# Kernel optimization log

Hardware: AMD Instinct MI355X
Metric: run time of the kernel (lower is better)

## Reference

```python
import jax, jax.numpy as jnp
import numpy as np

BN_EPS = 1e-5

def conv1x1(x, w, b):
    # x: [B, Cin, L], w: [Cout, Cin], b: [Cout] -> [B, Cout, L]
    return jnp.einsum('bcl,oc->bol', x, w) + b[None, :, None]

def maxpool2(x):
    # x: [B, C, L] -> [B, C, L//2], kernel=stride=2
    B, C, L = x.shape
    return x.reshape(B, C, L // 2, 2).max(axis=-1)

def setup_inputs() -> dict:
    key = jax.random.key(0)
    ks = jax.random.split(key, 12)
    B, C, L = 8, 512, 4096
    Ci = C // 2
    s_in = 1.0 / np.sqrt(C)
    s_mid = 1.0 / np.sqrt(Ci)
    return {
        'x':       jax.random.normal(ks[0], (B, C, L), jnp.float32),
        'theta_w': jax.random.uniform(ks[1], (Ci, C), jnp.float32, -s_in, s_in),
        'theta_b': jax.random.uniform(ks[2], (Ci,), jnp.float32, -s_in, s_in),
        'phi_w':   jax.random.uniform(ks[3], (Ci, C), jnp.float32, -s_in, s_in),
        'phi_b':   jax.random.uniform(ks[4], (Ci,), jnp.float32, -s_in, s_in),
        'g_w':     jax.random.uniform(ks[5], (Ci, C), jnp.float32, -s_in, s_in),
        'g_b':     jax.random.uniform(ks[6], (Ci,), jnp.float32, -s_in, s_in),
        'wz_w':    jax.random.uniform(ks[7], (C, Ci), jnp.float32, -s_mid, s_mid),
        'wz_b':    jax.random.uniform(ks[8], (C,), jnp.float32, -s_mid, s_mid),
        'bn_gamma': jax.random.normal(ks[9], (C,), jnp.float32),
        'bn_beta':  jax.random.normal(ks[10], (C,), jnp.float32),
    }

def reference(x, theta_w, theta_b, phi_w, phi_b, g_w, g_b, wz_w, wz_b, bn_gamma, bn_beta):
    B, C, L = x.shape
    Ci = C // 2
    # projections
    theta = conv1x1(x, theta_w, theta_b)                 # [B, Ci, L]
    phi   = maxpool2(conv1x1(x, phi_w, phi_b))           # [B, Ci, L/2]
    g     = maxpool2(conv1x1(x, g_w, g_b))               # [B, Ci, L/2]
    # non-local attention (unscaled)
    f = jnp.einsum('bcq,bck->bqk', theta, phi)           # [B, L, L/2]
    f = jax.nn.softmax(f, axis=-1)
    y = jnp.einsum('bqk,bck->bcq', f, g)                 # [B, Ci, L]
    # wz: conv1x1 + BatchNorm1d (training mode: batch stats, biased var)
    z = conv1x1(y, wz_w, wz_b)                           # [B, C, L]
    mean = z.mean(axis=(0, 2))
    var = ((z - mean[None, :, None]) ** 2).mean(axis=(0, 2))
    z_hat = (z - mean[None, :, None]) * jax.lax.rsqrt(var + BN_EPS)[None, :, None]
    wz = z_hat * bn_gamma[None, :, None] + bn_beta[None, :, None]
    return wz + x
```

## Files before the change

### kernel.cpp

```cpp
#include <hip/hip_runtime.h>

#define BATCH 8
#define CIN   512
#define LEN   4096
#define CI    256
#define KLEN  2048

typedef _Float16 half_t;
typedef _Float16 half2_t __attribute__((ext_vector_type(2)));
typedef _Float16 half4_t __attribute__((ext_vector_type(4)));
typedef _Float16 half8_t __attribute__((ext_vector_type(8)));
typedef float    floatx4 __attribute__((ext_vector_type(4)));

__device__ __forceinline__ void async16(void* lds_dst, const void* g_src) {
    __builtin_amdgcn_global_load_lds(
        (const __attribute__((address_space(1))) unsigned int*)g_src,
        (__attribute__((address_space(3))) unsigned int*)lds_dst,
        16, 0, 0);
}

__global__ __launch_bounds__(256) void xpose_kernel(
    const float* __restrict__ x, half_t* __restrict__ xhT)
{
    __shared__ half_t tile[64][72];
    const int b = blockIdx.z, c0 = blockIdx.y * 64, l0 = blockIdx.x * 64;
    const int t = threadIdx.x;
    #pragma unroll
    for (int i = 0; i < 4; i++) {
        int fid = t + 256 * i;
        int c = fid >> 4, lb = (fid & 15) << 2;
        float4 v = *(const float4*)(x + ((size_t)b * CIN + c0 + c) * LEN + l0 + lb);
        tile[lb + 0][c] = (half_t)v.x;
        tile[lb + 1][c] = (half_t)v.y;
        tile[lb + 2][c] = (half_t)v.z;
        tile[lb + 3][c] = (half_t)v.w;
    }
    __syncthreads();
    #pragma unroll
    for (int i = 0; i < 2; i++) {
        int fid = t + 256 * i;
        int l = fid >> 3, cb = (fid & 7) << 3;
        half8_t v = *(const half8_t*)&tile[l][cb];
        *(half8_t*)(xhT + ((size_t)b * LEN + l0 + l) * CIN + c0 + cb) = v;
    }
}

__global__ __launch_bounds__(256) void wconv_kernel(
    const float* __restrict__ tw, const float* __restrict__ pw,
    const float* __restrict__ gw, const float* __restrict__ wzw,
    half_t* __restrict__ Wh, half_t* __restrict__ wzh)
{
    size_t base = ((size_t)blockIdx.x * 256 + threadIdx.x) * 8;
    const float* src;
    half_t* dst;
    if (base < 768 * 512) {
        size_t o = base >> 9, c = base & 511;
        src = (o < 256 ? tw + o * 512
                       : (o < 512 ? pw + (o - 256) * 512 : gw + (o - 512) * 512)) + c;
        dst = Wh + base;
    } else {
        size_t off = base - 768 * 512;
        src = wzw + off;
        dst = wzh + off;
    }
    float4 a = *(const float4*)src, b2 = *(const float4*)(src + 4);
    half8_t h = { (half_t)a.x, (half_t)a.y, (half_t)a.z, (half_t)a.w,
                  (half_t)b2.x, (half_t)b2.y, (half_t)b2.z, (half_t)b2.w };
    *(half8_t*)dst = h;
}

__global__ __launch_bounds__(256, 2) void projmm_kernel(
    const half_t* __restrict__ xhT, const half_t* __restrict__ Wh,
    const float* __restrict__ tb, const float* __restrict__ pb,
    const float* __restrict__ gb,
    half_t* __restrict__ thetaT, half_t* __restrict__ phiT,
    half_t* __restrict__ gperm)
{
    __shared__ half_t wsm[128 * 32];
    __shared__ half_t xsm[128 * 32];

    const int b  = blockIdx.z;
    const int o0 = blockIdx.y * 128;
    const int l0 = blockIdx.x * 128;
    const int t  = threadIdx.x;
    const int lane = t & 63, w = t >> 6;
    const int ln = lane & 15, quad = lane >> 4;
    const int wm = w >> 1, wn = w & 1;

    floatx4 acc[4][4];
    #pragma unroll
    for (int mi = 0; mi < 4; mi++)
        #pragma unroll
        for (int nj = 0; nj < 4; nj++) acc[mi][nj] = (floatx4)(0.0f);

    const half_t* Wb = Wh + (size_t)o0 * 512;
    const half_t* xb = xhT + ((size_t)b * LEN + l0) * CIN;

    for (int k0 = 0; k0 < 512; k0 += 32) {
        __syncthreads();
        #pragma unroll
        for (int it = 0; it < 2; it++) {
            int grp = w * 2 + it;
            async16(&wsm[grp * 512],
                    Wb + (size_t)(grp * 16 + ln) * 512 + k0 + quad * 8);
            async16(&xsm[grp * 512],
                    xb + (size_t)(grp * 16 + ln) * CIN + k0 + quad * 8);
        }
        __syncthreads();
        half8_t af[4], bf[4];
        #pragma unroll
        for (int mi = 0; mi < 4; mi++)
            af[mi] = *(const half8_t*)&wsm[(wm * 4 + mi) * 512 + lane * 8];
        #pragma unroll
        for (int nj = 0; nj < 4; nj++)
            bf[nj] = *(const half8_t*)&xsm[(wn * 4 + nj) * 512 + lane * 8];
        #pragma unroll
        for (int mi = 0; mi < 4; mi++)
            #pragma unroll
            for (int nj = 0; nj < 4; nj++)
                acc[mi][nj] = __builtin_amdgcn_mfma_f32_16x16x32_f16(
                                  af[mi], bf[nj], acc[mi][nj], 0, 0, 0);
    }

    const int which = o0 >> 8;
    const int obase = o0 & 255;
    const float* Bp = which == 0 ? tb : (which == 1 ? pb : gb);

    float bias[4][4];
    #pragma unroll
    for (int mi = 0; mi < 4; mi++)
        #pragma unroll
        for (int r = 0; r < 4; r++)
            bias[mi][r] = Bp[obase + wm * 64 + mi * 16 + quad * 4 + r];

    if (which == 0) {
        #pragma unroll
        for (int mi = 0; mi < 4; mi++) {
            int o = obase + wm * 64 + mi * 16 + quad * 4;
            #pragma unroll
            for (int nj = 0; nj < 4; nj++) {
                int l = l0 + wn * 64 + nj * 16 + ln;
                half4_t v = { (half_t)(acc[mi][nj][0] + bias[mi][0]),
                              (half_t)(acc[mi][nj][1] + bias[mi][1]),
                              (half_t)(acc[mi][nj][2] + bias[mi][2]),
                              (half_t)(acc[mi][nj][3] + bias[mi][3]) };
                *(half4_t*)(thetaT + ((size_t)b * LEN + l) * CI + o) = v;
            }
        }
    } else {
        #pragma unroll
        for (int mi = 0; mi < 4; mi++) {
            int o = obase + wm * 64 + mi * 16 + quad * 4;
            #pragma unroll
            for (int nj = 0; nj < 4; nj++) {
                int l = l0 + wn * 64 + nj * 16 + ln;
                float mx[4];
                #pragma unroll
                for (int r = 0; r < 4; r++) {
                    float other = __shfl_xor(acc[mi][nj][r], 1);
                    mx[r] = fmaxf(acc[mi][nj][r], other) + bias[mi][r];
                }
                if ((ln & 1) == 0) {
                    int kk = l >> 1;
                    if (which == 1) {
                        half4_t v = { (half_t)mx[0], (half_t)mx[1],
                                      (half_t)mx[2], (half_t)mx[3] };
                        *(half4_t*)(phiT + ((size_t)b * KLEN + kk) * CI + o) = v;
                    } else {
                        int loc = kk & 63;
                        int v = ((loc >> 5) & 1) * 32 + ((loc >> 2) & 3) * 8
                              + ((loc >> 4) & 1) * 4 + (loc & 3);
                        int kdst = (kk & ~63) | v;
                        #pragma unroll
                        for (int r = 0; r < 4; r++)
                            gperm[((size_t)b * CI + o + r) * KLEN + kdst] =
                                (half_t)mx[r];
                    }
                }
            }
        }
    }
}

__global__ __launch_bounds__(256, 2) void attn_kernel(
    const half_t* __restrict__ thetaT,
    const half_t* __restrict__ phiT,
    const half_t* __restrict__ gperm,
    half_t* __restrict__ yhT)
{
    __shared__ half_t phi_s[64 * 256];
    __shared__ half_t g_s[256 * 64];

    const int b    = blockIdx.x;
    const int q0   = blockIdx.y * 64;
    const int t    = threadIdx.x;
    const int w    = t >> 6;
    const int lane = t & 63;
    const int ln   = lane & 15;
    const int quad = lane >> 4;
    const int qw   = q0 + w * 16;

    half8_t thf[8];
    {
        const half_t* thb = thetaT + ((size_t)b * LEN + qw + ln) * CI + quad * 8;
        #pragma unroll
        for (int ch = 0; ch < 8; ch++)
            thf[ch] = *(const half8_t*)(thb + ch * 32);
    }

    floatx4 O[16];
    #pragma unroll
    for (int i = 0; i < 16; i++) O[i] = (floatx4)(0.0f);
    float m_run = -3.0e38f;
    float l_run = 0.0f;

    const half_t* phib = phiT + (size_t)b * KLEN * CI;
    const half_t* gpb  = gperm + (size_t)b * CI * KLEN;

    for (int kt = 0; kt < KLEN; kt += 64) {
        __syncthreads();
        #pragma unroll
        for (int ii = 0; ii < 8; ii++) {
            int grp = w * 8 + ii;
            int k16 = grp >> 3, ch = grp & 7;
            async16(&phi_s[grp * 512],
                    phib + (size_t)(kt + k16 * 16 + ln) * CI + ch * 32 + quad * 8);
        }
        #pragma unroll
        for (int ii = 0; ii < 8; ii++) {
            int grp = w * 8 + ii;
            int tc = grp >> 4, csub = grp & 15;
            async16(&g_s[grp * 512],
                    gpb + (size_t)(csub * 16 + ln) * KLEN + kt + tc * 32 + quad * 8);
        }
        __syncthreads();

        floatx4 S[4];
        #pragma unroll
        for (int k16 = 0; k16 < 4; k16++) S[k16] = (floatx4)(0.0f);
        #pragma unroll
        for (int k16 = 0; k16 < 4; k16++)
            #pragma unroll
            for (int ch = 0; ch < 8; ch++) {
                half8_t a = *(const half8_t*)&phi_s[(k16 * 8 + ch) * 512 + lane * 8];
                S[k16] = __builtin_amdgcn_mfma_f32_16x16x32_f16(
                             a, thf[ch], S[k16], 0, 0, 0);
            }

        float tmax = S[0][0];
        #pragma unroll
        for (int k16 = 0; k16 < 4; k16++)
            #pragma unroll
            for (int r = 0; r < 4; r++) tmax = fmaxf(tmax, S[k16][r]);
        tmax = fmaxf(tmax, __shfl_xor(tmax, 16));
        tmax = fmaxf(tmax, __shfl_xor(tmax, 32));
        float m_new = fmaxf(m_run, tmax);
        float alpha = __expf(m_run - m_new);
        m_run = m_new;
        l_run *= alpha;

        float p[4][4];
        #pragma unroll
        for (int k16 = 0; k16 < 4; k16++) {
            #pragma unroll
            for (int r = 0; r < 4; r++) {
                p[k16][r] = __expf(S[k16][r] - m_new);
                l_run += p[k16][r];
            }
        }
        half8_t Pf[2];
        #pragma unroll
        for (int tc = 0; tc < 2; tc++) {
            half8_t pv = { (half_t)p[2*tc][0],   (half_t)p[2*tc][1],
                           (half_t)p[2*tc][2],   (half_t)p[2*tc][3],
                           (half_t)p[2*tc+1][0], (half_t)p[2*tc+1][1],
                           (half_t)p[2*tc+1][2], (half_t)p[2*tc+1][3] };
            Pf[tc] = pv;
        }
        #pragma unroll
        for (int i = 0; i < 16; i++) O[i] *= alpha;

        #pragma unroll
        for (int tc = 0; tc < 2; tc++)
            #pragma unroll
            for (int csub = 0; csub < 16; csub++) {
                half8_t a = *(const half8_t*)&g_s[(tc * 16 + csub) * 512 + lane * 8];
                O[csub] = __builtin_amdgcn_mfma_f32_16x16x32_f16(
                              a, Pf[tc], O[csub], 0, 0, 0);
            }
    }

    l_run += __shfl_xor(l_run, 16);
    l_run += __shfl_xor(l_run, 32);
    float inv = 1.0f / l_run;
    half_t* yb = yhT + ((size_t)b * LEN + qw + ln) * CI;
    #pragma unroll
    for (int csub = 0; csub < 16; csub++) {
        int c = csub * 16 + quad * 4;
        half4_t v = { (half_t)(O[csub][0] * inv), (half_t)(O[csub][1] * inv),
                      (half_t)(O[csub][2] * inv), (half_t)(O[csub][3] * inv) };
        *(half4_t*)(yb + c) = v;
    }
}

__global__ __launch_bounds__(256, 2) void zmm_kernel(
    const half_t* __restrict__ yhT, const half_t* __restrict__ wzh,
    const float* __restrict__ wzb, float* __restrict__ z,
    float* __restrict__ bns, float* __restrict__ bnq)
{
    __shared__ half_t ysm[128 * 32];
    __shared__ half_t wsm[128 * 32];

    const int b  = blockIdx.z;
    const int o0 = blockIdx.y * 128;
    const int l0 = blockIdx.x * 128;
    const int t  = threadIdx.x;
    const int lane = t & 63, w = t >> 6;
    const int ln = lane & 15, quad = lane >> 4;
    const int wm = w >> 1, wn = w & 1;

    floatx4 acc[4][4];
    #pragma unroll
    for (int mi = 0; mi < 4; mi++)
        #pragma unroll
        for (int nj = 0; nj < 4; nj++) acc[mi][nj] = (floatx4)(0.0f);

    const half_t* yb = yhT + ((size_t)b * LEN + l0) * CI;
    const half_t* Wb = wzh + (size_t)o0 * CI;

    for (int k0 = 0; k0 < 256; k0 += 32) {
        __syncthreads();
        #pragma unroll
        for (int it = 0; it < 2; it++) {
            int grp = w * 2 + it;
            async16(&ysm[grp * 512],
                    yb + (size_t)(grp * 16 + ln) * CI + k0 + quad * 8);
            async16(&wsm[grp * 512],
                    Wb + (size_t)(grp * 16 + ln) * CI + k0 + quad * 8);
        }
        __syncthreads();
        half8_t af[4], bf[4];
        #pragma unroll
        for (int mi = 0; mi < 4; mi++)
            af[mi] = *(const half8_t*)&ysm[(wm * 4 + mi) * 512 + lane * 8];
        #pragma unroll
        for (int nj = 0; nj < 4; nj++)
            bf[nj] = *(const half8_t*)&wsm[(wn * 4 + nj) * 512 + lane * 8];
        #pragma unroll
        for (int mi = 0; mi < 4; mi++)
            #pragma unroll
            for (int nj = 0; nj < 4; nj++)
                acc[mi][nj] = __builtin_amdgcn_mfma_f32_16x16x32_f16(
                                  af[mi], bf[nj], acc[mi][nj], 0, 0, 0);
    }

    float s[4] = {0, 0, 0, 0}, s2[4] = {0, 0, 0, 0};
    #pragma unroll
    for (int nj = 0; nj < 4; nj++) {
        int o = o0 + wn * 64 + nj * 16 + ln;
        float bo = wzb[o];
        #pragma unroll
        for (int mi = 0; mi < 4; mi++) {
            int l = l0 + wm * 64 + mi * 16 + quad * 4;
            float4 v = make_float4(acc[mi][nj][0] + bo, acc[mi][nj][1] + bo,
                                   acc[mi][nj][2] + bo, acc[mi][nj][3] + bo);
            *(float4*)(z + ((size_t)b * CIN + o) * LEN + l) = v;
            s[nj]  += (v.x + v.y) + (v.z + v.w);
            s2[nj] += (v.x * v.x + v.y * v.y) + (v.z * v.z + v.w * v.w);
        }
    }
    #pragma unroll
    for (int nj = 0; nj < 4; nj++) {
        float sv = s[nj], qv = s2[nj];
        sv += __shfl_xor(sv, 16); sv += __shfl_xor(sv, 32);
        qv += __shfl_xor(qv, 16); qv += __shfl_xor(qv, 32);
        if (quad == 0) {
            int o = o0 + wn * 64 + nj * 16 + ln;
            atomicAdd(&bns[o], sv);
            atomicAdd(&bnq[o], qv);
        }
    }
}

__global__ __launch_bounds__(256) void bn_kernel(
    float* __restrict__ z, const float* __restrict__ x,
    const float* __restrict__ bns, const float* __restrict__ bnq,
    const float* __restrict__ gamma, const float* __restrict__ beta)
{
    size_t i4 = (size_t)blockIdx.x * 256 + threadIdx.x;
    size_t base = i4 << 2;
    int c = (int)((base >> 12) & (CIN - 1));
    const float invn = 1.0f / (BATCH * LEN);
    float mean = bns[c] * invn;
    float var  = bnq[c] * invn - mean * mean;
    float sc = gamma[c] * rsqrtf(var + 1e-5f);
    float sh = beta[c] - mean * sc;
    float4 zv = *(const float4*)(z + base);
    float4 xv = *(const float4*)(x + base);
    float4 o;
    o.x = zv.x * sc + sh + xv.x;
    o.y = zv.y * sc + sh + xv.y;
    o.z = zv.z * sc + sh + xv.z;
    o.w = zv.w * sc + sh + xv.w;
    *(float4*)(z + base) = o;
}

extern "C" void kernel_launch(void* const* d_in, const int* in_sizes, int n_in,
                              void* d_out, int out_size, void* d_ws, size_t ws_size,
                              hipStream_t stream)
{
    const float* x     = (const float*)d_in[0];
    const float* tw    = (const float*)d_in[1];
    const float* tb    = (const float*)d_in[2];
    const float* pw    = (const float*)d_in[3];
    const float* pb    = (const float*)d_in[4];
    const float* gw    = (const float*)d_in[5];
    const float* gb    = (const float*)d_in[6];
    const float* wzw   = (const float*)d_in[7];
    const float* wzb   = (const float*)d_in[8];
    const float* gamma = (const float*)d_in[9];
    const float* beta  = (const float*)d_in[10];

    float* out = (float*)d_out;

    half_t* xhT    = (half_t*)d_ws;
    half_t* thetaT = xhT    + (size_t)BATCH * LEN * CIN;
    half_t* phiT   = thetaT + (size_t)BATCH * LEN * CI;
    half_t* gperm  = phiT   + (size_t)BATCH * KLEN * CI;
    half_t* yhT    = gperm  + (size_t)BATCH * CI * KLEN;
    half_t* Wh     = yhT    + (size_t)BATCH * LEN * CI;
    half_t* wzh    = Wh     + (size_t)768 * 512;
    float*  bns    = (float*)(wzh + (size_t)512 * 256);
    float*  bnq    = bns + CIN;

    hipMemsetAsync(bns, 0, 2 * CIN * sizeof(float), stream);

    wconv_kernel<<<256, 256, 0, stream>>>(tw, pw, gw, wzw, Wh, wzh);

    xpose_kernel<<<dim3(LEN / 64, CIN / 64, BATCH), 256, 0, stream>>>(x, xhT);

    projmm_kernel<<<dim3(LEN / 128, 6, BATCH), 256, 0, stream>>>(
        xhT, Wh, tb, pb, gb, thetaT, phiT, gperm);

    attn_kernel<<<dim3(BATCH, LEN / 64), 256, 0, stream>>>(
        thetaT, phiT, gperm, yhT);

    zmm_kernel<<<dim3(LEN / 128, CIN / 128, BATCH), 256, 0, stream>>>(
        yhT, wzh, wzb, out, bns, bnq);

    bn_kernel<<<(BATCH * CIN * LEN) / 4 / 256, 256, 0, stream>>>(
        out, x, bns, bnq, gamma, beta);
}
```

Measured before the change: 367.6 us.

## Pre-tile g into MFMA fragment layout, load directly to registers, swizzle phi LDS

The projection kernel now writes g in a per-64-key tile layout that matches the MFMA A-fragment order. The attention kernel can then load g fragments straight from global memory into registers, with double-buffered register sets, instead of staging them through LDS. The phi LDS tile is stored row-major with an XOR-style rotation to avoid bank conflicts. The projection and z GEMM loaders switch to row-contiguous coalesced async loads. This cuts LDS traffic and footprint in the attention loop, which may improve occupancy, but it raises register pressure and makes performance depend on global-load latency for g.

```diff
diff --git a/kernel.cpp b/kernel.cpp
--- a/kernel.cpp
+++ b/kernel.cpp
@@ -100,20 +100,19 @@
         __syncthreads();
         #pragma unroll
         for (int it = 0; it < 2; it++) {
-            int grp = w * 2 + it;
-            async16(&wsm[grp * 512],
-                    Wb + (size_t)(grp * 16 + ln) * 512 + k0 + quad * 8);
-            async16(&xsm[grp * 512],
-                    xb + (size_t)(grp * 16 + ln) * CIN + k0 + quad * 8);
+            int off = t * 16 + it * 4096;
+            int row = off >> 6, c8 = (off >> 4) & 3;
+            async16(&wsm[off >> 1], Wb + (size_t)row * 512 + k0 + c8 * 8);
+            async16(&xsm[off >> 1], xb + (size_t)row * CIN + k0 + c8 * 8);
         }
         __syncthreads();
         half8_t af[4], bf[4];
         #pragma unroll
         for (int mi = 0; mi < 4; mi++)
-            af[mi] = *(const half8_t*)&wsm[(wm * 4 + mi) * 512 + lane * 8];
+            af[mi] = *(const half8_t*)&wsm[(wm * 64 + mi * 16 + ln) * 32 + quad * 8];
         #pragma unroll
         for (int nj = 0; nj < 4; nj++)
-            bf[nj] = *(const half8_t*)&xsm[(wn * 4 + nj) * 512 + lane * 8];
+            bf[nj] = *(const half8_t*)&xsm[(wn * 64 + nj * 16 + ln) * 32 + quad * 8];
         #pragma unroll
         for (int mi = 0; mi < 4; mi++)
             #pragma unroll
@@ -150,7 +149,7 @@
     } else {
         #pragma unroll
         for (int mi = 0; mi < 4; mi++) {
-            int o = obase + wm * 64 + mi * 16 + quad * 4;
+            int ob4 = obase + wm * 64 + mi * 16 + quad * 4;
             #pragma unroll
             for (int nj = 0; nj < 4; nj++) {
                 int l = l0 + wn * 64 + nj * 16 + ln;
@@ -165,16 +164,22 @@
                     if (which == 1) {
                         half4_t v = { (half_t)mx[0], (half_t)mx[1],
                                       (half_t)mx[2], (half_t)mx[3] };
-                        *(half4_t*)(phiT + ((size_t)b * KLEN + kk) * CI + o) = v;
+                        *(half4_t*)(phiT + ((size_t)b * KLEN + kk) * CI + ob4) = v;
                     } else {
-                        int loc = kk & 63;
-                        int v = ((loc >> 5) & 1) * 32 + ((loc >> 2) & 3) * 8
-                              + ((loc >> 4) & 1) * 4 + (loc & 3);
-                        int kdst = (kk & ~63) | v;
+                        int ktile = kk >> 6, kl = kk & 63;
+                        int tc  = kl >> 5;
+                        int h16 = (kl >> 4) & 1;
+                        int qd  = (kl & 15) >> 2;
+                        int j   = h16 * 4 + (kl & 3);
+                        size_t base = (size_t)b * (CI * KLEN)
+                                    + (size_t)ktile * 16384 + tc * 8192 + j;
                         #pragma unroll
-                        for (int r = 0; r < 4; r++)
-                            gperm[((size_t)b * CI + o + r) * KLEN + kdst] =
+                        for (int r = 0; r < 4; r++) {
+                            int c = ob4 + r;
+                            int csub = c >> 4, lnc = c & 15;
+                            gperm[base + csub * 512 + (qd * 16 + lnc) * 8] =
                                 (half_t)mx[r];
+                        }
                     }
                 }
             }
@@ -189,7 +194,6 @@
     half_t* __restrict__ yhT)
 {
     __shared__ half_t phi_s[64 * 256];
-    __shared__ half_t g_s[256 * 64];
 
     const int b    = blockIdx.x;
     const int q0   = blockIdx.y * 64;
@@ -215,37 +219,39 @@
     float l_run = 0.0f;
 
     const half_t* phib = phiT + (size_t)b * KLEN * CI;
-    const half_t* gpb  = gperm + (size_t)b * CI * KLEN;
-
-    for (int kt = 0; kt < KLEN; kt += 64) {
-        __syncthreads();
-        #pragma unroll
-        for (int ii = 0; ii < 8; ii++) {
-            int grp = w * 8 + ii;
-            int k16 = grp >> 3, ch = grp & 7;
-            async16(&phi_s[grp * 512],
-                    phib + (size_t)(kt + k16 * 16 + ln) * CI + ch * 32 + quad * 8);
-        }
-        #pragma unroll
-        for (int ii = 0; ii < 8; ii++) {
-            int grp = w * 8 + ii;
-            int tc = grp >> 4, csub = grp & 15;
-            async16(&g_s[grp * 512],
-                    gpb + (size_t)(csub * 16 + ln) * KLEN + kt + tc * 32 + quad * 8);
-        }
+    const half_t* gpb  = gperm + (size_t)b * (CI * KLEN);
+
+    for (int kt = 0; kt < 32; kt++) {
+        __syncthreads();
+        #pragma unroll
+        for (int it = 0; it < 8; it++) {
+            int o = t * 16 + it * 4096;
+            int row = o >> 9, slot = (o >> 4) & 31;
+            int gsrc = (slot - 4 * row) & 31;
+            async16(&phi_s[o >> 1],
+                    phib + (size_t)(kt * 64 + row) * CI + gsrc * 8);
+        }
+        const half_t* gkt = gpb + (size_t)kt * 16384;
+        half8_t gfa[8], gfb[8];
+        #pragma unroll
+        for (int cs = 0; cs < 8; cs++)
+            gfa[cs] = *(const half8_t*)(gkt + cs * 512 + lane * 8);
         __syncthreads();
 
         floatx4 S[4];
         #pragma unroll
         for (int k16 = 0; k16 < 4; k16++) S[k16] = (floatx4)(0.0f);
         #pragma unroll
-        for (int k16 = 0; k16 < 4; k16++)
+        for (int k16 = 0; k16 < 4; k16++) {
+            int row = k16 * 16 + ln;
             #pragma unroll
             for (int ch = 0; ch < 8; ch++) {
-                half8_t a = *(const half8_t*)&phi_s[(k16 * 8 + ch) * 512 + lane * 8];
+                int slot = (ch * 4 + quad + 4 * ln) & 31;
+                half8_t a = *(const half8_t*)&phi_s[row * 256 + slot * 8];
                 S[k16] = __builtin_amdgcn_mfma_f32_16x16x32_f16(
                              a, thf[ch], S[k16], 0, 0, 0);
             }
+        }
 
         float tmax = S[0][0];
         #pragma unroll
@@ -261,13 +267,12 @@
 
         float p[4][4];
         #pragma unroll
-        for (int k16 = 0; k16 < 4; k16++) {
+        for (int k16 = 0; k16 < 4; k16++)
             #pragma unroll
             for (int r = 0; r < 4; r++) {
                 p[k16][r] = __expf(S[k16][r] - m_new);
                 l_run += p[k16][r];
             }
-        }
         half8_t Pf[2];
         #pragma unroll
         for (int tc = 0; tc < 2; tc++) {
@@ -281,13 +286,30 @@
         for (int i = 0; i < 16; i++) O[i] *= alpha;
 
         #pragma unroll
-        for (int tc = 0; tc < 2; tc++)
-            #pragma unroll
-            for (int csub = 0; csub < 16; csub++) {
-                half8_t a = *(const half8_t*)&g_s[(tc * 16 + csub) * 512 + lane * 8];
-                O[csub] = __builtin_amdgcn_mfma_f32_16x16x32_f16(
-                              a, Pf[tc], O[csub], 0, 0, 0);
-            }
+        for (int cs = 0; cs < 8; cs++)
+            gfb[cs] = *(const half8_t*)(gkt + (8 + cs) * 512 + lane * 8);
+        #pragma unroll
+        for (int cs = 0; cs < 8; cs++)
+            O[cs] = __builtin_amdgcn_mfma_f32_16x16x32_f16(
+                        gfa[cs], Pf[0], O[cs], 0, 0, 0);
+        #pragma unroll
+        for (int cs = 0; cs < 8; cs++)
+            gfa[cs] = *(const half8_t*)(gkt + (16 + cs) * 512 + lane * 8);
+        #pragma unroll
+        for (int cs = 0; cs < 8; cs++)
+            O[8 + cs] = __builtin_amdgcn_mfma_f32_16x16x32_f16(
+                            gfb[cs], Pf[0], O[8 + cs], 0, 0, 0);
+        #pragma unroll
+        for (int cs = 0; cs < 8; cs++)
+            gfb[cs] = *(const half8_t*)(gkt + (24 + cs) * 512 + lane * 8);
+        #pragma unroll
+        for (int cs = 0; cs < 8; cs++)
+            O[cs] = __builtin_amdgcn_mfma_f32_16x16x32_f16(
+                        gfa[cs], Pf[1], O[cs], 0, 0, 0);
+        #pragma unroll
+        for (int cs = 0; cs < 8; cs++)
+            O[8 + cs] = __builtin_amdgcn_mfma_f32_16x16x32_f16(
+                            gfb[cs], Pf[1], O[8 + cs], 0, 0, 0);
     }
 
     l_run += __shfl_xor(l_run, 16);
@@ -332,20 +354,19 @@
         __syncthreads();
         #pragma unroll
         for (int it = 0; it < 2; it++) {
-            int grp = w * 2 + it;
-            async16(&ysm[grp * 512],
-                    yb + (size_t)(grp * 16 + ln) * CI + k0 + quad * 8);
-            async16(&wsm[grp * 512],
-                    Wb + (size_t)(grp * 16 + ln) * CI + k0 + quad * 8);
+            int off = t * 16 + it * 4096;
+            int row = off >> 6, c8 = (off >> 4) & 3;
+            async16(&ysm[off >> 1], yb + (size_t)row * CI + k0 + c8 * 8);
+            async16(&wsm[off >> 1], Wb + (size_t)row * CI + k0 + c8 * 8);
         }
         __syncthreads();
         half8_t af[4], bf[4];
         #pragma unroll
         for (int mi = 0; mi < 4; mi++)
-            af[mi] = *(const half8_t*)&ysm[(wm * 4 + mi) * 512 + lane * 8];
+            af[mi] = *(const half8_t*)&ysm[(wm * 64 + mi * 16 + ln) * 32 + quad * 8];
         #pragma unroll
         for (int nj = 0; nj < 4; nj++)
-            bf[nj] = *(const half8_t*)&wsm[(wn * 4 + nj) * 512 + lane * 8];
+            bf[nj] = *(const half8_t*)&wsm[(wn * 64 + nj * 16 + ln) * 32 + quad * 8];
         #pragma unroll
         for (int mi = 0; mi < 4; mi++)
             #pragma unroll
```

Measured after the change: 341.3 us. 1.08x faster.
